# Kernel optimization log

Hardware: AMD Instinct MI355X
Metric: run time of the kernel (lower is better)

Reference implementation:

```python
import jax, jax.numpy as jnp
import numpy as np

BIT_SIZE = 8
ES_SIZE = 1
IN_F = 2048
OUT_F = 2048
N = 8192


def posit_quantize(x, nbits, es):
    """Round-to-nearest posit(nbits, es) quantization, returned as float32.

    Posit value: sign * useed^k * 2^e * (1+f), useed = 2^(2^es).
    Regime length rlen = k+2 (k>=0) or -k+1 (k<0); fraction bits =
    nbits - 1(sign) - rlen - es, clamped at 0. Magnitudes are clamped to
    [minpos, maxpos] (posits never round a nonzero value to zero/inf).
    """
    two_es = 2 ** es                      # useed = 2**two_es
    npat = nbits - 2
    maxpos = jnp.float32(2.0 ** (two_es * npat))
    minpos = jnp.float32(2.0 ** (-two_es * npat))

    sign = jnp.sign(x)
    ax = jnp.clip(jnp.abs(x), minpos, maxpos)

    s = jnp.floor(jnp.log2(ax))           # integer power-of-two scale
    k = jnp.floor(s / two_es)             # regime value
    rlen = jnp.where(k >= 0, k + 2.0, -k + 1.0)
    fbits = jnp.maximum(nbits - 1.0 - rlen - es, 0.0)

    m = ax * jnp.exp2(-s)                 # mantissa in [1, 2)
    fscale = jnp.exp2(fbits)
    mq = jnp.round(m * fscale) / fscale   # round fraction to fbits
    # carry: mantissa rounded up to 2.0 -> bump exponent
    s = jnp.where(mq >= 2.0, s + 1.0, s)
    mq = jnp.where(mq >= 2.0, 1.0, mq)

    y = sign * mq * jnp.exp2(s)
    y = jnp.clip(y, -maxpos, maxpos)
    return jnp.where(x == 0, jnp.float32(0.0), y).astype(x.dtype)


def setup_inputs() -> dict:
    key = jax.random.key(0)
    kx, kw, kb = jax.random.split(key, 3)
    x = jax.random.normal(kx, (N, IN_F), dtype=jnp.float32)
    bound = 1.0 / np.sqrt(IN_F)  # nn.Linear default init range
    weight = jax.random.uniform(kw, (OUT_F, IN_F), dtype=jnp.float32,
                                minval=-bound, maxval=bound)
    bias = jax.random.uniform(kb, (OUT_F,), dtype=jnp.float32,
                              minval=-bound, maxval=bound)
    return {"x": x, "weight": weight, "bias": bias}


def reference(x, weight, bias):
    xq = posit_quantize(x, BIT_SIZE, ES_SIZE)
    wq = posit_quantize(weight, BIT_SIZE, ES_SIZE)
    bq = posit_quantize(bias, BIT_SIZE, ES_SIZE)
    # y = xq @ wq^T + bq  (nn.Linear)
    return jnp.einsum('ni,oi->no', xq, wq) + bq
```

## Files before the change

kernel.cpp:

```cpp
#include <hip/hip_runtime.h>

typedef __attribute__((ext_vector_type(8))) short bf16x8;
typedef __attribute__((ext_vector_type(4))) float f32x4;

__device__ __forceinline__ float posit_q(float x) {
  float ax = fabsf(x);
  ax = fmaxf(ax, 0x1p-12f);
  ax = fminf(ax, 0x1p12f);
  int s = (int)(__float_as_uint(ax) >> 23) - 127;
  int k = s >> 1;
  int rlen = (k >= 0) ? (k + 2) : (1 - k);
  int fbits = 6 - rlen;
  fbits = fbits < 0 ? 0 : fbits;
  float m = ax * __uint_as_float((unsigned)(127 - s) << 23);
  float fs = (float)(1 << fbits);
  float inv_fs = __uint_as_float((unsigned)(127 - fbits) << 23);
  float mq = rintf(m * fs) * inv_fs;
  if (mq >= 2.0f) { s += 1; mq = 1.0f; }
  float y = mq * __uint_as_float((unsigned)(127 + s) << 23);
  y = fminf(y, 0x1p12f);
  y = copysignf(y, x);
  return (x == 0.0f) ? 0.0f : y;
}

__device__ __forceinline__ ushort4 quant4_bf16(float4 v) {
  ushort4 o;
  o.x = (ushort)(__float_as_uint(posit_q(v.x)) >> 16);
  o.y = (ushort)(__float_as_uint(posit_q(v.y)) >> 16);
  o.z = (ushort)(__float_as_uint(posit_q(v.z)) >> 16);
  o.w = (ushort)(__float_as_uint(posit_q(v.w)) >> 16);
  return o;
}

__global__ void posit_quant_all(const float* __restrict__ x,
                                const float* __restrict__ w,
                                const float* __restrict__ b,
                                ushort* __restrict__ Xq,
                                ushort* __restrict__ Wq,
                                float* __restrict__ bq,
                                int nx4, int nw4, int nb4) {
  int i = blockIdx.x * blockDim.x + threadIdx.x;
  if (i < nx4) {
    ((ushort4*)Xq)[i] = quant4_bf16(((const float4*)x)[i]);
  } else if (i < nx4 + nw4) {
    int j = i - nx4;
    ((ushort4*)Wq)[j] = quant4_bf16(((const float4*)w)[j]);
  } else if (i < nx4 + nw4 + nb4) {
    int j = i - nx4 - nw4;
    float4 v = ((const float4*)b)[j];
    float4 o;
    o.x = posit_q(v.x); o.y = posit_q(v.y);
    o.z = posit_q(v.z); o.w = posit_q(v.w);
    ((float4*)bq)[j] = o;
  }
}

__device__ __forceinline__ void gl_lds16(const ushort* g, ushort* l) {
  __builtin_amdgcn_global_load_lds(
      (const __attribute__((address_space(1))) void*)g,
      (__attribute__((address_space(3))) void*)l,
      16, 0, 0);
}

__global__ __launch_bounds__(512, 4) void posit_gemm(
    const ushort* __restrict__ A, const ushort* __restrict__ B,
    const float* __restrict__ bq, float* __restrict__ C,
    int M, int N, int K) {
  __shared__ ushort sA[256 * 64];
  __shared__ ushort sB[128 * 64];

  const int tid = threadIdx.x;
  const int wave = tid >> 6;
  const int lane = tid & 63;
  const int wm = wave >> 1;
  const int wn = wave & 1;
  const int m0 = blockIdx.y << 8;
  const int n0 = blockIdx.x << 7;

  const int g8 = lane >> 3;
  const int qe = ((lane & 7) ^ g8) << 3;
  const int rb = (wave << 3) + g8;

  const ushort* Ag = A + (size_t)(m0 + rb) * K + qe;
  const ushort* Bg = B + (size_t)(n0 + rb) * K + qe;
  const size_t rstep = (size_t)64 * K;

  const int wbase = wave << 9;
  ushort* lA0 = sA + wbase;
  ushort* lB0 = sB + wbase;

  const int fr = lane & 15;
  const int t4 = lane >> 4;
  const int pk0 = ((t4 ^ (fr & 7)) << 3);
  const int pk1 = (((4 + t4) ^ (fr & 7)) << 3);

  f32x4 acc[4][4];
#pragma unroll
  for (int i = 0; i < 4; i++)
#pragma unroll
    for (int j = 0; j < 4; j++) acc[i][j] = (f32x4){0.f, 0.f, 0.f, 0.f};

  for (int k0 = 0; k0 < K; k0 += 64) {
#pragma unroll
    for (int r = 0; r < 4; r++)
      gl_lds16(Ag + k0 + r * rstep, lA0 + (r << 12));
#pragma unroll
    for (int r = 0; r < 2; r++)
      gl_lds16(Bg + k0 + r * rstep, lB0 + (r << 12));
    __syncthreads();

#pragma unroll
    for (int kk = 0; kk < 2; kk++) {
      const int pk = kk ? pk1 : pk0;
      bf16x8 fa[4], fb[4];
#pragma unroll
      for (int i = 0; i < 4; i++)
        fa[i] = *(const bf16x8*)(sA + (((wm << 6) + (i << 4) + fr) << 6) + pk);
#pragma unroll
      for (int j = 0; j < 4; j++)
        fb[j] = *(const bf16x8*)(sB + (((wn << 6) + (j << 4) + fr) << 6) + pk);

#pragma unroll
      for (int i = 0; i < 4; i++)
#pragma unroll
        for (int j = 0; j < 4; j++)
          acc[i][j] = __builtin_amdgcn_mfma_f32_16x16x32_bf16(
              fa[i], fb[j], acc[i][j], 0, 0, 0);
    }
    __syncthreads();
  }

  const int row0 = m0 + (wm << 6) + (t4 << 2);
  const int col0 = n0 + (wn << 6) + fr;
#pragma unroll
  for (int j = 0; j < 4; j++) {
    const int col = col0 + (j << 4);
    const float bv = bq[col];
#pragma unroll
    for (int i = 0; i < 4; i++) {
      const int row = row0 + (i << 4);
#pragma unroll
      for (int r = 0; r < 4; r++)
        C[(size_t)(row + r) * N + col] = acc[i][j][r] + bv;
    }
  }
}

extern "C" void kernel_launch(void* const* d_in, const int* in_sizes, int n_in,
                              void* d_out, int out_size, void* d_ws, size_t ws_size,
                              hipStream_t stream) {
  const float* x = (const float*)d_in[0];
  const float* w = (const float*)d_in[1];
  const float* bias = (const float*)d_in[2];
  float* out = (float*)d_out;

  const int out_f = in_sizes[2];
  const int in_f = in_sizes[1] / out_f;
  const int m = in_sizes[0] / in_f;
  const int k = in_f;

  ushort* Xq = (ushort*)d_ws;
  ushort* Wq = Xq + (size_t)m * k;
  float* bquant = (float*)(Wq + (size_t)out_f * k);

  const int nx4 = in_sizes[0] / 4;
  const int nw4 = in_sizes[1] / 4;
  const int nb4 = in_sizes[2] / 4;
  const int total4 = nx4 + nw4 + nb4;
  posit_quant_all<<<(total4 + 255) / 256, 256, 0, stream>>>(
      x, w, bias, Xq, Wq, bquant, nx4, nw4, nb4);

  dim3 grid(out_f / 128, m / 256);
  posit_gemm<<<grid, 512, 0, stream>>>(Xq, Wq, bquant, out, m, out_f, k);
}
```

Baseline: 184.7 us.

## Prefetch next K tile into registers while computing current tile

```diff
diff --git a/kernel.cpp b/kernel.cpp
--- a/kernel.cpp
+++ b/kernel.cpp
@@ -55,13 +55,6 @@
   }
 }
 
-__device__ __forceinline__ void gl_lds16(const ushort* g, ushort* l) {
-  __builtin_amdgcn_global_load_lds(
-      (const __attribute__((address_space(1))) void*)g,
-      (__attribute__((address_space(3))) void*)l,
-      16, 0, 0);
-}
-
 __global__ __launch_bounds__(512, 4) void posit_gemm(
     const ushort* __restrict__ A, const ushort* __restrict__ B,
     const float* __restrict__ bq, float* __restrict__ C,
@@ -85,9 +78,8 @@
   const ushort* Bg = B + (size_t)(n0 + rb) * K + qe;
   const size_t rstep = (size_t)64 * K;
 
-  const int wbase = wave << 9;
-  ushort* lA0 = sA + wbase;
-  ushort* lB0 = sB + wbase;
+  ushort* la = sA + (wave << 9) + (lane << 3);
+  ushort* lb = sB + (wave << 9) + (lane << 3);
 
   const int fr = lane & 15;
   const int t4 = lane >> 4;
@@ -100,14 +92,33 @@
 #pragma unroll
     for (int j = 0; j < 4; j++) acc[i][j] = (f32x4){0.f, 0.f, 0.f, 0.f};
 
-  for (int k0 = 0; k0 < K; k0 += 64) {
+  bf16x8 pfA[4], pfB[2];
+
+  auto loadregs = [&](int k0) {
 #pragma unroll
     for (int r = 0; r < 4; r++)
-      gl_lds16(Ag + k0 + r * rstep, lA0 + (r << 12));
+      pfA[r] = *(const bf16x8*)(Ag + k0 + r * rstep);
 #pragma unroll
     for (int r = 0; r < 2; r++)
-      gl_lds16(Bg + k0 + r * rstep, lB0 + (r << 12));
-    __syncthreads();
+      pfB[r] = *(const bf16x8*)(Bg + k0 + r * rstep);
+  };
+
+  auto writeregs = [&]() {
+#pragma unroll
+    for (int r = 0; r < 4; r++)
+      *(bf16x8*)(la + (r << 12)) = pfA[r];
+#pragma unroll
+    for (int r = 0; r < 2; r++)
+      *(bf16x8*)(lb + (r << 12)) = pfB[r];
+  };
+
+  loadregs(0);
+  writeregs();
+  __syncthreads();
+
+  for (int k0 = 0; k0 < K; k0 += 64) {
+    const bool more = (k0 + 64) < K;
+    if (more) loadregs(k0 + 64);
 
 #pragma unroll
     for (int kk = 0; kk < 2; kk++) {
@@ -128,6 +139,10 @@
               fa[i], fb[j], acc[i][j], 0, 0, 0);
     }
     __syncthreads();
+    if (more) {
+      writeregs();
+      __syncthreads();
+    }
   }
 
   const int row0 = m0 + (wm << 6) + (t4 << 2);
```

Result: slower. 193.9 us (+5.0%).
